# Optimization experiments

Measured on AMD Instinct MI355X. Metric: run time of the kernel, lower is better.

## Reference

```python
import jax, jax.numpy as jnp
import numpy as np

B, S, IN_F, OUT_F = 4, 2048, 4096, 4096

def setup_inputs() -> dict:
    key = jax.random.key(0)
    k1, k2, k3 = jax.random.split(key, 3)
    # int8 activations and weights (symmetric range)
    x = jax.random.randint(k1, (B, S, IN_F), -128, 128, dtype=jnp.int32).astype(jnp.int8)
    weight_q = jax.random.randint(k2, (OUT_F, IN_F), -128, 128, dtype=jnp.int32).astype(jnp.int8)
    scale_x = jnp.float32(0.05)   # activation quant scale
    scale_w = jnp.float32(0.02)   # weight quant scale (scalar, per-tensor)
    scale_y = jax.random.uniform(k3, (OUT_F,), minval=0.5, maxval=2.0, dtype=jnp.float32)  # per-output-row scale
    return {"x": x, "weight_q": weight_q, "scale_x": scale_x, "scale_w": scale_w, "scale_y": scale_y}

def reference(x, weight_q, scale_x, scale_w, scale_y):
    # int8 GEMM with int32 accumulation: [B,S,IN] @ [OUT,IN]^T -> [B,S,OUT]
    acc = jax.lax.dot_general(x, weight_q, ((((2,), (1,)), ((), ()))),
                              preferred_element_type=jnp.int32)
    # fused requantization scale: scale_x * scale_w / scale_y  -> [OUT]
    requant_scale = (scale_x * scale_w / scale_y).astype(jnp.float32)
    out_f = acc.astype(jnp.float32) * requant_scale  # broadcast over last dim
    out_q = jnp.clip(jnp.round(out_f), -128, 127).astype(jnp.int8)
    return out_q, scale_y
```

## Files before the change

kernel.cpp:

```cpp
#include <hip/hip_runtime.h>
#include <cstdint>


#define MDIM 8192
#define NDIM 4096
#define KDIM 4096
#define BM 256
#define BN 256
#define BKB 128
#define NT (KDIM / BKB)

typedef int v4i __attribute__((ext_vector_type(4)));

#define FENCE() asm volatile("" ::: "memory")
#define BAR()                     \
  do {                            \
    FENCE();                      \
    __builtin_amdgcn_s_barrier(); \
    FENCE();                      \
  } while (0)

__device__ __forceinline__ uint32_t pack4(int a, int b, int c, int d) {
  return (uint32_t)(a & 0xFF) | ((uint32_t)(b & 0xFF) << 8) |
         ((uint32_t)(c & 0xFF) << 16) | ((uint32_t)(d & 0xFF) << 24);
}

__global__ __launch_bounds__(256) void pack_kernel(
    const int* __restrict__ x32, const int* __restrict__ w32,
    const float* __restrict__ sy, uint8_t* __restrict__ x8f,
    uint8_t* __restrict__ w8f, float* __restrict__ tail) {
  const int t = blockIdx.x * 256 + threadIdx.x;
  if (t < NDIM) tail[t] = sy[t];
  const int NXC = (MDIM / 16) * KDIM;
  const int NWC = (NDIM / 16) * KDIM;
  if (t >= NXC + NWC) return;
  const int* src;
  uint8_t* dst;
  int chunk;
  if (t < NXC) {
    chunk = t;
    src = x32;
    dst = x8f;
  } else {
    chunk = t - NXC;
    src = w32;
    dst = w8f;
  }
  const int blk = chunk >> 11;
  const int cb = chunk & 2047;
  const int mb = blk >> 5;
  const int kt = blk & 31;
  const int region = cb >> 6;
  const int lpos = cb & 63;
  const int kh = region >> 4, rf = region & 15;
  const int kl = lpos >> 4, fr = lpos & 15;
  const int r = mb * 256 + rf * 16 + fr;
  const int k0 = kt * 128 + kh * 64 + kl * 16;
  const int* s = src + (size_t)r * KDIM + k0;
  v4i a0 = *(const v4i*)(s + 0);
  v4i a1 = *(const v4i*)(s + 4);
  v4i a2 = *(const v4i*)(s + 8);
  v4i a3 = *(const v4i*)(s + 12);
  v4i o;
  o[0] = (int)pack4(a0[0], a0[1], a0[2], a0[3]);
  o[1] = (int)pack4(a1[0], a1[1], a1[2], a1[3]);
  o[2] = (int)pack4(a2[0], a2[1], a2[2], a2[3]);
  o[3] = (int)pack4(a3[0], a3[1], a3[2], a3[3]);
  *(v4i*)(dst + (size_t)chunk * 16) = o;
}

__global__ __launch_bounds__(512, 2) void gemm_kernel(
    const uint8_t* __restrict__ A8, const uint8_t* __restrict__ B8,
    const float* __restrict__ sxp, const float* __restrict__ swp,
    const float* __restrict__ syp, float* __restrict__ out) {
  __shared__ __align__(16) uint8_t lds[131072];

  const int tid = threadIdx.x;
  const int lane = tid & 63;
  const int wave = tid >> 6;

  const int wg = ((int)blockIdx.x % 8) * 64 + (int)blockIdx.x / 8;
  const int mb = wg >> 4;
  const int nb = wg & 15;

  const int wm2 = wave >> 2;
  const int wn4 = wave & 3;

  const uint8_t* Abase = A8 + ((size_t)(mb * 32) << 15);
  const uint8_t* Bbase = B8 + ((size_t)(nb * 32) << 15);

  const uint32_t sdst = (uint32_t)tid * 16;
  const uint32_t lane16 = (uint32_t)lane * 16;
  const uint32_t aoff = (uint32_t)(wm2 * 8) << 10;
  const uint32_t boff = (uint32_t)(wn4 * 4) << 10;

  v4i acc[8][4];
#pragma unroll
  for (int i = 0; i < 8; i++)
#pragma unroll
    for (int j = 0; j < 4; j++) acc[i][j] = (v4i){0, 0, 0, 0};

  auto gload = [&](const uint8_t* src, uint32_t ldsoff) {
    __builtin_amdgcn_global_load_lds(
        (const __attribute__((address_space(1))) void*)src,
        (__attribute__((address_space(3))) void*)(lds + ldsoff), 16, 0, 0);
  };
  auto stage = [&](int t) {
    const uint32_t lb = (uint32_t)(t & 1) * 65536u + sdst;
    const uint8_t* sa = Abase + ((size_t)t << 15) + sdst;
    const uint8_t* sb = Bbase + ((size_t)t << 15) + sdst;
#pragma unroll
    for (int r = 0; r < 4; ++r) {
      gload(sa + r * 8192, lb + r * 8192);
      gload(sb + r * 8192, lb + 32768u + r * 8192);
    }
  };

  stage(0);

  for (int t = 0; t < NT; ++t) {
    asm volatile("s_waitcnt vmcnt(0)" ::: "memory");
    BAR();
    if (t + 1 < NT) stage(t + 1);

    const uint8_t* LA = lds + (uint32_t)(t & 1) * 65536u;
    const uint8_t* LB = LA + 32768u;

    v4i af0[8], bf0[4], af1[8], bf1[4];
#pragma unroll
    for (int j = 0; j < 4; j++)
      bf0[j] = *(const v4i*)(LB + boff + (j << 10) + lane16);
#pragma unroll
    for (int i = 0; i < 8; i++)
      af0[i] = *(const v4i*)(LA + aoff + (i << 10) + lane16);
#pragma unroll
    for (int j = 0; j < 4; j++)
      bf1[j] = *(const v4i*)(LB + 16384u + boff + (j << 10) + lane16);
#pragma unroll
    for (int i = 0; i < 8; i++)
      af1[i] = *(const v4i*)(LA + 16384u + aoff + (i << 10) + lane16);

#pragma unroll
    for (int i = 0; i < 8; i++)
#pragma unroll
      for (int j = 0; j < 4; j++)
        acc[i][j] =
            __builtin_amdgcn_mfma_i32_16x16x64_i8(af0[i], bf0[j], acc[i][j], 0, 0, 0);
#pragma unroll
    for (int i = 0; i < 8; i++)
#pragma unroll
      for (int j = 0; j < 4; j++)
        acc[i][j] =
            __builtin_amdgcn_mfma_i32_16x16x64_i8(af1[i], bf1[j], acc[i][j], 0, 0, 0);
  }

  const float s = sxp[0] * swp[0];
  const int kl = lane >> 4;
  const int fr = lane & 15;
  const int wrow = mb * 256 + wm2 * 128;
  const int wcol = nb * 256 + wn4 * 64;
#pragma unroll
  for (int j = 0; j < 4; j++) {
    const int col = wcol + j * 16 + fr;
    const float rs = s / syp[col];
#pragma unroll
    for (int i = 0; i < 8; i++) {
      const int row0 = wrow + i * 16 + kl * 4;
#pragma unroll
      for (int r = 0; r < 4; r++) {
        float v = rintf((float)acc[i][j][r] * rs);
        v = fminf(127.f, fmaxf(-128.f, v));
        out[(size_t)(row0 + r) * NDIM + col] = v;
      }
    }
  }
}

extern "C" void kernel_launch(void* const* d_in, const int* in_sizes, int n_in,
                              void* d_out, int out_size, void* d_ws, size_t ws_size,
                              hipStream_t stream) {
  const int* x32 = (const int*)d_in[0];
  const int* w32 = (const int*)d_in[1];
  const float* sx = (const float*)d_in[2];
  const float* sw = (const float*)d_in[3];
  const float* sy = (const float*)d_in[4];
  float* out = (float*)d_out;
  float* tail = out + (size_t)MDIM * NDIM;

  uint8_t* x8f = (uint8_t*)d_ws;
  uint8_t* w8f = x8f + (size_t)MDIM * KDIM;

  const int total = (MDIM / 16) * KDIM + (NDIM / 16) * KDIM;
  pack_kernel<<<total / 256, 256, 0, stream>>>(x32, w32, sy, x8f, w8f, tail);

  const int nblocks = (MDIM / BM) * (NDIM / BN);
  gemm_kernel<<<nblocks, 512, 0, stream>>>(x8f, w8f, sx, sw, sy, out);
}
```

Measured before the change: 185.8 us.

## Give each wave private LDS staging and drop block barriers in int8 GEMM

Restructures the GEMM so each of 4 waves computes a 128x128 tile and streams its own A/B slices into a private double-buffered LDS region via global_load_lds, removing block-wide barriers. The packing kernel layout is changed to 64-wide K chunks laid out per 128-row wave slice. This removes barrier stalls and enlarges the per-wave MFMA tile, but duplicates global/LDS traffic across waves sharing rows or columns and lowers occupancy to 4 waves per block with 1 block per CU.

```diff
diff --git a/kernel.cpp b/kernel.cpp
--- a/kernel.cpp
+++ b/kernel.cpp
@@ -7,18 +7,9 @@
 #define KDIM 4096
 #define BM 256
 #define BN 256
-#define BKB 128
-#define NT (KDIM / BKB)
+#define NH 64
 
 typedef int v4i __attribute__((ext_vector_type(4)));
-
-#define FENCE() asm volatile("" ::: "memory")
-#define BAR()                     \
-  do {                            \
-    FENCE();                      \
-    __builtin_amdgcn_s_barrier(); \
-    FENCE();                      \
-  } while (0)
 
 __device__ __forceinline__ uint32_t pack4(int a, int b, int c, int d) {
   return (uint32_t)(a & 0xFF) | ((uint32_t)(b & 0xFF) << 8) |
@@ -46,16 +37,13 @@
     src = w32;
     dst = w8f;
   }
-  const int blk = chunk >> 11;
-  const int cb = chunk & 2047;
-  const int mb = blk >> 5;
-  const int kt = blk & 31;
-  const int region = cb >> 6;
-  const int lpos = cb & 63;
-  const int kh = region >> 4, rf = region & 15;
+  const int lpos = chunk & 63;
+  const int rf = (chunk >> 6) & 15;
+  const int h = (chunk >> 10) & 63;
+  const int mb = chunk >> 16;
   const int kl = lpos >> 4, fr = lpos & 15;
   const int r = mb * 256 + rf * 16 + fr;
-  const int k0 = kt * 128 + kh * 64 + kl * 16;
+  const int k0 = h * 64 + kl * 16;
   const int* s = src + (size_t)r * KDIM + k0;
   v4i a0 = *(const v4i*)(s + 0);
   v4i a1 = *(const v4i*)(s + 4);
@@ -69,7 +57,7 @@
   *(v4i*)(dst + (size_t)chunk * 16) = o;
 }
 
-__global__ __launch_bounds__(512, 2) void gemm_kernel(
+__global__ __launch_bounds__(256, 1) void gemm_kernel(
     const uint8_t* __restrict__ A8, const uint8_t* __restrict__ B8,
     const float* __restrict__ sxp, const float* __restrict__ swp,
     const float* __restrict__ syp, float* __restrict__ out) {
@@ -83,84 +71,73 @@
   const int mb = wg >> 4;
   const int nb = wg & 15;
 
-  const int wm2 = wave >> 2;
-  const int wn4 = wave & 3;
+  const int wm2 = wave >> 1;
+  const int wn2 = wave & 1;
 
-  const uint8_t* Abase = A8 + ((size_t)(mb * 32) << 15);
-  const uint8_t* Bbase = B8 + ((size_t)(nb * 32) << 15);
+  const uint8_t* Asrc = A8 + ((size_t)mb << 20) + ((size_t)wm2 << 13);
+  const uint8_t* Bsrc = B8 + ((size_t)nb << 20) + ((size_t)wn2 << 13);
 
-  const uint32_t sdst = (uint32_t)tid * 16;
+  uint8_t* wlds = lds + wave * 32768;
   const uint32_t lane16 = (uint32_t)lane * 16;
-  const uint32_t aoff = (uint32_t)(wm2 * 8) << 10;
-  const uint32_t boff = (uint32_t)(wn4 * 4) << 10;
 
-  v4i acc[8][4];
+  v4i acc[8][8];
 #pragma unroll
   for (int i = 0; i < 8; i++)
 #pragma unroll
-    for (int j = 0; j < 4; j++) acc[i][j] = (v4i){0, 0, 0, 0};
+    for (int j = 0; j < 8; j++) acc[i][j] = (v4i){0, 0, 0, 0};
 
-  auto gload = [&](const uint8_t* src, uint32_t ldsoff) {
+  auto gload = [&](const uint8_t* src, uint8_t* ldst) {
     __builtin_amdgcn_global_load_lds(
         (const __attribute__((address_space(1))) void*)src,
-        (__attribute__((address_space(3))) void*)(lds + ldsoff), 16, 0, 0);
+        (__attribute__((address_space(3))) void*)ldst, 16, 0, 0);
   };
-  auto stage = [&](int t) {
-    const uint32_t lb = (uint32_t)(t & 1) * 65536u + sdst;
-    const uint8_t* sa = Abase + ((size_t)t << 15) + sdst;
-    const uint8_t* sb = Bbase + ((size_t)t << 15) + sdst;
+  auto stage = [&](int h) {
+    const uint32_t rb = (uint32_t)(h & 1) * 16384u;
+    const uint8_t* sa = Asrc + ((size_t)h << 14) + lane16;
+    const uint8_t* sb = Bsrc + ((size_t)h << 14) + lane16;
+    uint8_t* la = wlds + rb + lane16;
 #pragma unroll
-    for (int r = 0; r < 4; ++r) {
-      gload(sa + r * 8192, lb + r * 8192);
-      gload(sb + r * 8192, lb + 32768u + r * 8192);
+    for (int r = 0; r < 8; ++r) {
+      gload(sa + r * 1024, la + r * 1024);
+      gload(sb + r * 1024, la + 8192 + r * 1024);
     }
   };
 
   stage(0);
 
-  for (int t = 0; t < NT; ++t) {
-    asm volatile("s_waitcnt vmcnt(0)" ::: "memory");
-    BAR();
-    if (t + 1 < NT) stage(t + 1);
+  for (int h = 0; h < NH; ++h) {
+    if (h + 1 < NH) {
+      stage(h + 1);
+      asm volatile("s_waitcnt vmcnt(16)" ::: "memory");
+    } else {
+      asm volatile("s_waitcnt vmcnt(0)" ::: "memory");
+    }
+    const uint8_t* LA = wlds + (uint32_t)(h & 1) * 16384u;
+    const uint8_t* LB = LA + 8192;
 
-    const uint8_t* LA = lds + (uint32_t)(t & 1) * 65536u;
-    const uint8_t* LB = LA + 32768u;
-
-    v4i af0[8], bf0[4], af1[8], bf1[4];
-#pragma unroll
-    for (int j = 0; j < 4; j++)
-      bf0[j] = *(const v4i*)(LB + boff + (j << 10) + lane16);
+    v4i af[8], bf[8];
 #pragma unroll
     for (int i = 0; i < 8; i++)
-      af0[i] = *(const v4i*)(LA + aoff + (i << 10) + lane16);
+      af[i] = *(const v4i*)(LA + (i << 10) + lane16);
 #pragma unroll
-    for (int j = 0; j < 4; j++)
-      bf1[j] = *(const v4i*)(LB + 16384u + boff + (j << 10) + lane16);
-#pragma unroll
-    for (int i = 0; i < 8; i++)
-      af1[i] = *(const v4i*)(LA + 16384u + aoff + (i << 10) + lane16);
+    for (int j = 0; j < 8; j++)
+      bf[j] = *(const v4i*)(LB + (j << 10) + lane16);
 
 #pragma unroll
     for (int i = 0; i < 8; i++)
 #pragma unroll
-      for (int j = 0; j < 4; j++)
+      for (int j = 0; j < 8; j++)
         acc[i][j] =
-            __builtin_amdgcn_mfma_i32_16x16x64_i8(af0[i], bf0[j], acc[i][j], 0, 0, 0);
-#pragma unroll
-    for (int i = 0; i < 8; i++)
-#pragma unroll
-      for (int j = 0; j < 4; j++)
-        acc[i][j] =
-            __builtin_amdgcn_mfma_i32_16x16x64_i8(af1[i], bf1[j], acc[i][j], 0, 0, 0);
+            __builtin_amdgcn_mfma_i32_16x16x64_i8(af[i], bf[j], acc[i][j], 0, 0, 0);
   }
 
   const float s = sxp[0] * swp[0];
   const int kl = lane >> 4;
   const int fr = lane & 15;
   const int wrow = mb * 256 + wm2 * 128;
-  const int wcol = nb * 256 + wn4 * 64;
+  const int wcol = nb * 256 + wn2 * 128;
 #pragma unroll
-  for (int j = 0; j < 4; j++) {
+  for (int j = 0; j < 8; j++) {
     const int col = wcol + j * 16 + fr;
     const float rs = s / syp[col];
 #pragma unroll
@@ -194,5 +171,5 @@
   pack_kernel<<<total / 256, 256, 0, stream>>>(x32, w32, sy, x8f, w8f, tail);
 
   const int nblocks = (MDIM / BM) * (NDIM / BN);
-  gemm_kernel<<<nblocks, 512, 0, stream>>>(x8f, w8f, sx, sw, sy, out);
+  gemm_kernel<<<nblocks, 256, 0, stream>>>(x8f, w8f, sx, sw, sy, out);
 }
```

Measured after the change: 207.2 us. 11.5% more time.

## Interleave per-k-half global prefetch with MFMA phases using fine-grained barriers

Applied to the files above, without the earlier changes.

Changes the packed layout so each 64-wide k-half of a tile is contiguous. The main loop is rewritten to split each k-step into two halves and four MFMA phases. Each phase issues one slice of the next tile's global-to-LDS load, waits on partial vmcnt, and raises wave priority around the MFMA bursts. This is meant to overlap global loads with compute and lower register pressure from fragment loads, at the cost of many more barriers per iteration.

```diff
diff --git a/kernel.cpp b/kernel.cpp
--- a/kernel.cpp
+++ b/kernel.cpp
@@ -7,17 +7,21 @@
 #define KDIM 4096
 #define BM 256
 #define BN 256
-#define BKB 128
-#define NT (KDIM / BKB)
+#define NT 32
 
 typedef int v4i __attribute__((ext_vector_type(4)));
 
 #define FENCE() asm volatile("" ::: "memory")
-#define BAR()                     \
+#define BARX()                    \
   do {                            \
     FENCE();                      \
     __builtin_amdgcn_s_barrier(); \
     FENCE();                      \
+  } while (0)
+#define LGKM0()                                        \
+  do {                                                 \
+    asm volatile("s_waitcnt lgkmcnt(0)" ::: "memory"); \
+    __builtin_amdgcn_sched_barrier(0);                 \
   } while (0)
 
 __device__ __forceinline__ uint32_t pack4(int a, int b, int c, int d) {
@@ -46,16 +50,13 @@
     src = w32;
     dst = w8f;
   }
-  const int blk = chunk >> 11;
-  const int cb = chunk & 2047;
-  const int mb = blk >> 5;
-  const int kt = blk & 31;
-  const int region = cb >> 6;
-  const int lpos = cb & 63;
-  const int kh = region >> 4, rf = region & 15;
+  const int lpos = chunk & 63;
+  const int rf = (chunk >> 6) & 15;
+  const int h = (chunk >> 10) & 63;
+  const int mb = chunk >> 16;
   const int kl = lpos >> 4, fr = lpos & 15;
   const int r = mb * 256 + rf * 16 + fr;
-  const int k0 = kt * 128 + kh * 64 + kl * 16;
+  const int k0 = h * 64 + kl * 16;
   const int* s = src + (size_t)r * KDIM + k0;
   v4i a0 = *(const v4i*)(s + 0);
   v4i a1 = *(const v4i*)(s + 4);
@@ -86,10 +87,10 @@
   const int wm2 = wave >> 2;
   const int wn4 = wave & 3;
 
-  const uint8_t* Abase = A8 + ((size_t)(mb * 32) << 15);
-  const uint8_t* Bbase = B8 + ((size_t)(nb * 32) << 15);
-
-  const uint32_t sdst = (uint32_t)tid * 16;
+  const uint8_t* Abase = A8 + ((size_t)mb << 20);
+  const uint8_t* Bbase = B8 + ((size_t)nb << 20);
+
+  const uint32_t tid16 = (uint32_t)tid * 16;
   const uint32_t lane16 = (uint32_t)lane * 16;
   const uint32_t aoff = (uint32_t)(wm2 * 8) << 10;
   const uint32_t boff = (uint32_t)(wn4 * 4) << 10;
@@ -105,53 +106,96 @@
         (const __attribute__((address_space(1))) void*)src,
         (__attribute__((address_space(3))) void*)(lds + ldsoff), 16, 0, 0);
   };
-  auto stage = [&](int t) {
-    const uint32_t lb = (uint32_t)(t & 1) * 65536u + sdst;
-    const uint8_t* sa = Abase + ((size_t)t << 15) + sdst;
-    const uint8_t* sb = Bbase + ((size_t)t << 15) + sdst;
-#pragma unroll
-    for (int r = 0; r < 4; ++r) {
-      gload(sa + r * 8192, lb + r * 8192);
-      gload(sb + r * 8192, lb + 32768u + r * 8192);
+  auto stage1 = [&](int t, int kh, int r) {
+    const uint8_t* src = (r < 2 ? Abase : Bbase) + ((size_t)(2 * t + kh) << 14) +
+                         (uint32_t)((r & 1) * 8192) + tid16;
+    const uint32_t dst = (uint32_t)(t & 1) * 65536u + (uint32_t)kh * 32768u +
+                         (uint32_t)((r >> 1) * 16384 + (r & 1) * 8192) + tid16;
+    gload(src, dst);
+  };
+
+#pragma unroll
+  for (int r = 0; r < 4; ++r) stage1(0, 0, r);
+#pragma unroll
+  for (int r = 0; r < 4; ++r) stage1(0, 1, r);
+  asm volatile("s_waitcnt vmcnt(4)" ::: "memory");
+  BARX();
+
+  for (int t = 0; t < NT; ++t) {
+    const bool pre = (t + 1 < NT);
+#pragma unroll
+    for (int kh = 0; kh < 2; ++kh) {
+      const uint8_t* SA = lds + (uint32_t)(t & 1) * 65536u + (uint32_t)kh * 32768u;
+      const uint8_t* SB = SA + 16384u;
+      v4i af[4], ag[4], bf[4];
+
+#pragma unroll
+      for (int i = 0; i < 4; ++i)
+        af[i] = *(const v4i*)(SA + aoff + (i << 10) + lane16);
+#pragma unroll
+      for (int j = 0; j < 2; ++j)
+        bf[j] = *(const v4i*)(SB + boff + (j << 10) + lane16);
+      if (pre) stage1(t + 1, kh, 0);
+      BARX();
+      LGKM0();
+      __builtin_amdgcn_s_setprio(1);
+#pragma unroll
+      for (int i = 0; i < 4; ++i)
+#pragma unroll
+        for (int j = 0; j < 2; ++j)
+          acc[i][j] =
+              __builtin_amdgcn_mfma_i32_16x16x64_i8(af[i], bf[j], acc[i][j], 0, 0, 0);
+      __builtin_amdgcn_s_setprio(0);
+      BARX();
+
+#pragma unroll
+      for (int j = 2; j < 4; ++j)
+        bf[j] = *(const v4i*)(SB + boff + (j << 10) + lane16);
+      if (pre) stage1(t + 1, kh, 1);
+      BARX();
+      LGKM0();
+      __builtin_amdgcn_s_setprio(1);
+#pragma unroll
+      for (int i = 0; i < 4; ++i)
+#pragma unroll
+        for (int j = 2; j < 4; ++j)
+          acc[i][j] =
+              __builtin_amdgcn_mfma_i32_16x16x64_i8(af[i], bf[j], acc[i][j], 0, 0, 0);
+      __builtin_amdgcn_s_setprio(0);
+      BARX();
+
+#pragma unroll
+      for (int i = 0; i < 4; ++i)
+        ag[i] = *(const v4i*)(SA + aoff + ((4 + i) << 10) + lane16);
+      if (pre) stage1(t + 1, kh, 2);
+      BARX();
+      LGKM0();
+      __builtin_amdgcn_s_setprio(1);
+#pragma unroll
+      for (int i = 0; i < 4; ++i)
+#pragma unroll
+        for (int j = 2; j < 4; ++j)
+          acc[4 + i][j] =
+              __builtin_amdgcn_mfma_i32_16x16x64_i8(ag[i], bf[j], acc[4 + i][j], 0, 0, 0);
+      __builtin_amdgcn_s_setprio(0);
+      BARX();
+
+      if (pre) stage1(t + 1, kh, 3);
+      BARX();
+      __builtin_amdgcn_s_setprio(1);
+#pragma unroll
+      for (int i = 0; i < 4; ++i)
+#pragma unroll
+        for (int j = 0; j < 2; ++j)
+          acc[4 + i][j] =
+              __builtin_amdgcn_mfma_i32_16x16x64_i8(ag[i], bf[j], acc[4 + i][j], 0, 0, 0);
+      __builtin_amdgcn_s_setprio(0);
+      if (pre)
+        asm volatile("s_waitcnt vmcnt(4)" ::: "memory");
+      else if (kh == 0)
+        asm volatile("s_waitcnt vmcnt(0)" ::: "memory");
+      BARX();
     }
-  };
-
-  stage(0);
-
-  for (int t = 0; t < NT; ++t) {
-    asm volatile("s_waitcnt vmcnt(0)" ::: "memory");
-    BAR();
-    if (t + 1 < NT) stage(t + 1);
-
-    const uint8_t* LA = lds + (uint32_t)(t & 1) * 65536u;
-    const uint8_t* LB = LA + 32768u;
-
-    v4i af0[8], bf0[4], af1[8], bf1[4];
-#pragma unroll
-    for (int j = 0; j < 4; j++)
-      bf0[j] = *(const v4i*)(LB + boff + (j << 10) + lane16);
-#pragma unroll
-    for (int i = 0; i < 8; i++)
-      af0[i] = *(const v4i*)(LA + aoff + (i << 10) + lane16);
-#pragma unroll
-    for (int j = 0; j < 4; j++)
-      bf1[j] = *(const v4i*)(LB + 16384u + boff + (j << 10) + lane16);
-#pragma unroll
-    for (int i = 0; i < 8; i++)
-      af1[i] = *(const v4i*)(LA + 16384u + aoff + (i << 10) + lane16);
-
-#pragma unroll
-    for (int i = 0; i < 8; i++)
-#pragma unroll
-      for (int j = 0; j < 4; j++)
-        acc[i][j] =
-            __builtin_amdgcn_mfma_i32_16x16x64_i8(af0[i], bf0[j], acc[i][j], 0, 0, 0);
-#pragma unroll
-    for (int i = 0; i < 8; i++)
-#pragma unroll
-      for (int j = 0; j < 4; j++)
-        acc[i][j] =
-            __builtin_amdgcn_mfma_i32_16x16x64_i8(af1[i], bf1[j], acc[i][j], 0, 0, 0);
   }
 
   const float s = sxp[0] * swp[0];
```

New measurement: 184.4 us. Within noise of the previous version (-0.7%).
